# Optimization experiments

Measured on AMD Instinct MI355X. Metric: run time of the kernel, lower is better.

The kernel has to match this reference:

```python
import jax, jax.numpy as jnp
import numpy as np

D_MODEL = 5
NUM_PRED = 3
D_K = D_MODEL + NUM_PRED  # 8
HIDDEN = 128
GRID_LEN = 0.1
NUM_GRIDS = 100  # time_horizon / grid_length
SCALE = float(np.power(D_K, 0.5))
OH = np.eye(NUM_PRED, dtype=np.float32)
ONEHOT_M = jnp.asarray(OH[0])   # mental predicate 0
ONEHOT_A1 = jnp.asarray(OH[1])  # action predicate 1
ONEHOT_A2 = jnp.asarray(OH[2])  # action predicate 2


def time_emb(t):
    # positional-style embedding: even dims sin, odd dims cos (matches fast_time_embedding)
    i = jnp.arange(D_MODEL)
    ang = jnp.asarray(t)[..., None] / (10000.0 ** (2.0 * i / D_MODEL))
    return jnp.where(i % 2 == 0, jnp.sin(ang), jnp.cos(ang))


def setup_inputs() -> dict:
    key = jax.random.key(0)
    ks = jax.random.split(key, 11)
    B, L = 1024, 2048
    times_a1 = jnp.sort(jax.random.uniform(ks[0], (B, L)) * 10.0, axis=1)
    times_a2 = jnp.sort(jax.random.uniform(ks[1], (B, L)) * 10.0, axis=1)
    u = jax.random.uniform(ks[2], (B, NUM_GRIDS))
    s = 0.05
    return {
        'times_a1': times_a1,
        'times_a2': times_a2,
        'u': u,
        'W_ih': s * jax.random.normal(ks[3], (4 * HIDDEN, 21)),
        'W_hh': s * jax.random.normal(ks[4], (4 * HIDDEN, HIDDEN)),
        'b_ih': s * jax.random.normal(ks[5], (4 * HIDDEN,)),
        'b_hh': s * jax.random.normal(ks[6], (4 * HIDDEN,)),
        'w1': s * jax.random.normal(ks[7], (5, HIDDEN)),
        'b1': s * jax.random.normal(ks[8], (5,)),
        'w2': s * jax.random.normal(ks[9], (1, 5)),
        'b2': s * jax.random.normal(ks[10], (1,)),
    }


def _forward(times_a1, times_a2, u, W_ih, W_hh, b_ih, b_hh, w1, b1, w2, b2):
    B = times_a1.shape[0]
    # action event embeddings: [B, L, D_MODEL+NUM_PRED]; k = v = concat over action types
    e1 = jnp.concatenate([time_emb(times_a1), jnp.broadcast_to(ONEHOT_A1, times_a1.shape + (NUM_PRED,))], axis=-1)
    e2 = jnp.concatenate([time_emb(times_a2), jnp.broadcast_to(ONEHOT_A2, times_a2.shape + (NUM_PRED,))], axis=-1)
    kv = jnp.concatenate([e1, e2], axis=1)  # [B, 2L, 8]

    cur_times = (jnp.arange(NUM_GRIDS) + 1.0) * GRID_LEN  # [100]

    def step(carry, xs):
        hx, cx, last_time, has_event, dyn_time = carry
        cur_time, u_t = xs
        # query for mental predicate 0 at cur_time: [8]
        q = jnp.concatenate([time_emb(cur_time), ONEHOT_M])
        scores = jnp.einsum('d,bld->bl', q, kv) / SCALE
        attn = jax.nn.softmax(scores, axis=-1)
        att_out = jnp.einsum('bl,bld->bd', attn, kv)  # [B, 8]
        # mental embedding: zeros before first event, else time-emb of last event + one-hot
        m_emb = jnp.concatenate([time_emb(last_time), jnp.broadcast_to(ONEHOT_M, (B, NUM_PRED))], axis=-1)
        m_emb = jnp.where(has_event[:, None], m_emb, 0.0)
        dyn_time = dyn_time + GRID_LEN
        ct_emb = time_emb(dyn_time)  # [B, 5]
        x = jnp.concatenate([att_out, m_emb, ct_emb], axis=-1)  # [B, 21]
        # torch LSTMCell: gates ordered i, f, g, o
        gates = x @ W_ih.T + hx @ W_hh.T + b_ih + b_hh
        i_, f_, g_, o_ = jnp.split(gates, 4, axis=-1)
        cx = jax.nn.sigmoid(f_) * cx + jax.nn.sigmoid(i_) * jnp.tanh(g_)
        hx = jax.nn.sigmoid(o_) * jnp.tanh(cx)
        hz = jax.nn.sigmoid((hx @ w1.T + b1) @ w2.T + b2)[:, 0]  # [B]
        # bernoulli(prob) with pre-drawn uniform; single mental predicate -> index always 0
        event = u_t < hz
        last_time = jnp.where(event, cur_time, last_time)
        has_event = has_event | event
        dyn_time = jnp.where(event, 0.0, dyn_time)
        return (hx, cx, last_time, has_event, dyn_time), (hz, event)

    init = (
        jnp.zeros((B, HIDDEN)), jnp.zeros((B, HIDDEN)),
        jnp.zeros((B,)), jnp.zeros((B,), dtype=bool), jnp.zeros((B,)),
    )
    _, (hazard, events) = jax.lax.scan(step, init, (cur_times, u.T))
    return hazard, events  # [NUM_GRIDS, B], [NUM_GRIDS, B]


def reference(times_a1, times_a2, u, W_ih, W_hh, b_ih, b_hh, w1, b1, w2, b2):
    return _forward(times_a1, times_a2, u, W_ih, W_hh, b_ih, b_hh, w1, b1, w2, b2)
```

## Files before the change

kernel.cpp:

```cpp
#include <hip/hip_runtime.h>
#include <math.h>

#define BTOT 1024
#define LEN  2048
#define T    100
#define HID  128

#define ATT_OFF_FLOATS 81920

#define C1 0.025118864315095794
#define C2 6.309573444801933e-04
#define C3 1.5848931924611134e-05
#define C4 3.9810717055349735e-07

#define TEMB(td) \
  float d0 = sinf((float)(td)); \
  float d1 = cosf((float)((td) * C1)); \
  float d2 = sinf((float)((td) * C2)); \
  float d3 = cosf((float)((td) * C3)); \
  float d4 = sinf((float)((td) * C4));

__device__ __forceinline__ float sig(float x) { return 1.0f / (1.0f + expf(-x)); }

using v2f = __attribute__((ext_vector_type(2))) float;
__device__ __forceinline__ v2f mkv2(float a, float b) { v2f r; r.x = a; r.y = b; return r; }

template <int CTRL>
__device__ __forceinline__ float dppadd(float x) {
  int r = __builtin_amdgcn_update_dpp(0, __float_as_int(x), CTRL, 0xF, 0xF, false);
  return x + __int_as_float(r);
}
__device__ __forceinline__ float wred(float x) {
  x = dppadd<0xB1>(x);
  x = dppadd<0x4E>(x);
  x = dppadd<0x124>(x);
  x = dppadd<0x128>(x);
  x += __shfl_xor(x, 16);
  x += __shfl_xor(x, 32);
  return x;
}
#define RED8(x) { x = dppadd<0xB1>(x); x = dppadd<0x4E>(x); x = dppadd<0x141>(x); }

__global__ void wprep_k(const float* __restrict__ Wih,
                        const float* __restrict__ Whh,
                        float4* __restrict__ wsT) {
  int i = blockIdx.x * 1024 + threadIdx.x;
  int g = i / 5120;
  int rem = i - g * 5120;
  int c = rem >> 10;
  int t2 = rem & 1023;
  int q = t2 >> 3, s = t2 & 7;
  int row = q + 128 * g;
  int E = 20 * s + 4 * c;
  float v[4];
#pragma unroll
  for (int k = 0; k < 4; k++) {
    int e = E + k;
    v[k] = (e < 21) ? Wih[row * 21 + e]
         : (e < 24) ? 0.f
         : (e < 152) ? Whh[row * HID + (e - 24)]
         : 0.f;
  }
  wsT[i] = make_float4(v[0], v[1], v[2], v[3]);
}

__global__ __attribute__((amdgpu_flat_work_group_size(512, 512)))
void attn_k(const float* __restrict__ ta1,
            const float* __restrict__ ta2,
            float* __restrict__ att) {
  const int b = blockIdx.x, tid = threadIdx.x;
  const int wave = tid >> 6, lane = tid & 63;

  __shared__ float qlds[T][8];
  __shared__ float strip[8][T][8];

  if (tid < T) {
    double ct = (double)(tid + 1) * 0.1;
    TEMB(ct);
    qlds[tid][0] = d0 * 0.35355339059327373f;
    qlds[tid][1] = d1 * 0.35355339059327373f;
    qlds[tid][2] = d2 * 0.35355339059327373f;
    qlds[tid][3] = d3 * 0.35355339059327373f;
    qlds[tid][4] = d4 * 0.35355339059327373f;
  }

#define E5(i) float e##i##_0, e##i##_1, e##i##_2, e##i##_3, e##i##_4;
  E5(0) E5(1) E5(2) E5(3) E5(4) E5(5) E5(6) E5(7)
#undef E5
#define STAGE(i, expr) { double td_ = (double)(expr); \
    e##i##_0 = sinf((float)td_); \
    e##i##_1 = cosf((float)(td_ * C1)); \
    e##i##_2 = sinf((float)(td_ * C2)); \
    e##i##_3 = cosf((float)(td_ * C3)); \
    e##i##_4 = sinf((float)(td_ * C4)); }
  STAGE(0, ta1[b * LEN + tid +    0])
  STAGE(1, ta1[b * LEN + tid +  512])
  STAGE(2, ta1[b * LEN + tid + 1024])
  STAGE(3, ta1[b * LEN + tid + 1536])
  STAGE(4, ta2[b * LEN + tid +    0])
  STAGE(5, ta2[b * LEN + tid +  512])
  STAGE(6, ta2[b * LEN + tid + 1024])
  STAGE(7, ta2[b * LEN + tid + 1536])
#undef STAGE
#define PIN5(i) asm volatile("" : "+v"(e##i##_0), "+v"(e##i##_1), \
    "+v"(e##i##_2), "+v"(e##i##_3), "+v"(e##i##_4));
  PIN5(0) PIN5(1) PIN5(2) PIN5(3) PIN5(4) PIN5(5) PIN5(6) PIN5(7)
#undef PIN5

  __syncthreads();

  for (int t = 0; t < T; t++) {
    const float4 qv = *(const float4*)&qlds[t][0];
    const float q4 = qlds[t][4];
    float Wx = 0.f, Wy = 0.f, Wz = 0.f, Ww = 0.f, W4 = 0.f, sA = 0.f, sB = 0.f;
#define EV(i, S) { \
    float s = fmaf(qv.x, e##i##_0, fmaf(qv.y, e##i##_1, \
              fmaf(qv.z, e##i##_2, fmaf(qv.w, e##i##_3, q4 * e##i##_4)))); \
    float e = __expf(s); S += e; \
    Wx = fmaf(e, e##i##_0, Wx); Wy = fmaf(e, e##i##_1, Wy); \
    Wz = fmaf(e, e##i##_2, Wz); Ww = fmaf(e, e##i##_3, Ww); \
    W4 = fmaf(e, e##i##_4, W4); }
    EV(0, sA) EV(1, sA) EV(2, sA) EV(3, sA)
    EV(4, sB) EV(5, sB) EV(6, sB) EV(7, sB)
#undef EV

    float r0 = wred(Wx), r1 = wred(Wy), r2 = wred(Wz), r3 = wred(Ww);
    float r4 = wred(W4), r5 = wred(sA), r6 = wred(sB);
    if (lane == 0) {
      *(float4*)&strip[wave][t][0] = make_float4(r0, r1, r2, r3);
      strip[wave][t][4] = r4; strip[wave][t][5] = r5; strip[wave][t][6] = r6;
    }
  }
  __syncthreads();

  if (tid < T) {
    float f0 = 0.f, f1 = 0.f, f2 = 0.f, f3 = 0.f, f4 = 0.f, f5 = 0.f, f6 = 0.f;
#pragma unroll
    for (int w = 0; w < 8; w++) {
      float4 a = *(float4*)&strip[w][tid][0];
      float4 bq = *(float4*)&strip[w][tid][4];
      f0 += a.x; f1 += a.y; f2 += a.z; f3 += a.w;
      f4 += bq.x; f5 += bq.y; f6 += bq.z;
    }
    float inv = 1.0f / (f5 + f6);
    float* o8 = &att[(size_t)b * (T * 8) + (size_t)tid * 8];
    o8[0] = f0 * inv; o8[1] = f1 * inv; o8[2] = f2 * inv;
    o8[3] = f3 * inv; o8[4] = f4 * inv;
    o8[5] = 0.f; o8[6] = f5 * inv; o8[7] = f6 * inv;
  }
}

#define XE(tb, b, e) (((tb) * 4 + (b)) * 160 + (e))

__global__ __attribute__((amdgpu_flat_work_group_size(1024, 1024)))
void lstm_k(const float* __restrict__ att,
            const float* __restrict__ u,
            const float4* __restrict__ wT,
            const float* __restrict__ bih,
            const float* __restrict__ bhh,
            const float* __restrict__ w1g,
            const float* __restrict__ b1g,
            const float* __restrict__ w2g,
            const float* __restrict__ b2g,
            float* __restrict__ out) {
  const int tid = threadIdx.x;
  const int bg = blockIdx.x * 4;
  const int s = tid & 7;
  const int q = tid >> 3;
  const int lane = tid & 63;
  const int s5 = s * 5;

  __shared__ float4 xls4[2][4][40];
  __shared__ float4 glds[4][128];
  __shared__ float red2[4][2];
  __shared__ float tembT[101][5];
  __shared__ float uT[4][100];
  __shared__ int stL[2][4], stD[2][4], stH[2][4];
  float* xf = (float*)xls4;

  const int chI = tid & 127;
  float bbc0 = bih[chI] + bhh[chI];
  float bbc1 = bih[chI + 128] + bhh[chI + 128];
  float bbc2 = bih[chI + 256] + bhh[chI + 256];
  float bbc3 = bih[chI + 384] + bhh[chI + 384];
  float wvc = 0.f;
#pragma unroll
  for (int j = 0; j < 5; j++) wvc = fmaf(w2g[j], w1g[j * HID + chI], wvc);
  float hconst = b2g[0];
#pragma unroll
  for (int j = 0; j < 5; j++) hconst = fmaf(w2g[j], b1g[j], hconst);
  asm volatile("" : "+v"(bbc0), "+v"(bbc1), "+v"(bbc2), "+v"(bbc3),
                    "+v"(wvc), "+v"(hconst));
  float cx = 0.f;

  for (int i = tid; i < 2 * 4 * 160; i += 1024) xf[i] = 0.f;
  if (tid < 101) {
    double td = (double)tid * 0.1;
    TEMB(td);
    tembT[tid][0] = d0; tembT[tid][1] = d1; tembT[tid][2] = d2;
    tembT[tid][3] = d3; tembT[tid][4] = d4;
  }
  for (int i = tid; i < 400; i += 1024) {
    int b = i / 100, tt = i - b * 100;
    uT[b][tt] = u[(size_t)(bg + b) * T + tt];
  }
  if (tid < 4) { stL[0][tid] = 0; stD[0][tid] = 0; stH[0][tid] = 0; }
  __syncthreads();

  if (tid < 32) {
    int b = tid >> 3, j = tid & 7;
    xf[XE(0, b, j)] = att[(size_t)(bg + b) * (T * 8) + j];
  } else if (tid >= 64 && tid < 84) {
    int s2 = tid - 64, b = s2 / 5, j = s2 % 5;
    xf[XE(0, b, 16 + j)] = tembT[1][j];
  }
  __syncthreads();

  const float4* wTp = wT;

#define FM1(g, b) \
  a##g##b = __builtin_elementwise_fma(mkv2(w##g.x, w##g.y), xlo, a##g##b); \
  a##g##b = __builtin_elementwise_fma(mkv2(w##g.z, w##g.w), xhi, a##g##b);

#define CHB(b, c) { \
    float4 xb = xls4[tb][b][s5 + (c)]; \
    v2f xlo = mkv2(xb.x, xb.y), xhi = mkv2(xb.z, xb.w); \
    FM1(0, b) FM1(1, b) FM1(2, b) FM1(3, b) }

#define CH(c) { \
    float4 w0 = wTp[(0 * 5 + (c)) * 1024 + tid]; \
    float4 w1 = wTp[(1 * 5 + (c)) * 1024 + tid]; \
    float4 w2 = wTp[(2 * 5 + (c)) * 1024 + tid]; \
    float4 w3 = wTp[(3 * 5 + (c)) * 1024 + tid]; \
    CHB(0, c) CHB(1, c) CHB(2, c) CHB(3, c) }

#define CALCEV(bb) \
    float z_ = hconst + red2[bb][0] + red2[bb][1]; \
    float hz_ = 1.f / (1.f + expf(-z_)); \
    int ev_ = (uT[bb][t] < hz_) ? 1 : 0; \
    int lastp_ = ev_ ? (t + 1) : stL[tb][bb]; \
    int hasp_ = stH[tb][bb] | ev_; \
    int dynp_ = ev_ ? 0 : (stD[tb][bb] + 1);

  for (int t = 0; t < T; t++) {
    const int tb = t & 1, tb1 = tb ^ 1;
    asm volatile("" : "+s"(wTp));

    v2f z2 = mkv2(0.f, 0.f);
    v2f a00 = z2, a01 = z2, a02 = z2, a03 = z2,
        a10 = z2, a11 = z2, a12 = z2, a13 = z2,
        a20 = z2, a21 = z2, a22 = z2, a23 = z2,
        a30 = z2, a31 = z2, a32 = z2, a33 = z2;
    CH(0) CH(1) CH(2) CH(3) CH(4)

    float h00 = a00.x + a00.y, h01 = a01.x + a01.y, h02 = a02.x + a02.y, h03 = a03.x + a03.y;
    float h10 = a10.x + a10.y, h11 = a11.x + a11.y, h12 = a12.x + a12.y, h13 = a13.x + a13.y;
    float h20 = a20.x + a20.y, h21 = a21.x + a21.y, h22 = a22.x + a22.y, h23 = a23.x + a23.y;
    float h30 = a30.x + a30.y, h31 = a31.x + a31.y, h32 = a32.x + a32.y, h33 = a33.x + a33.y;
    RED8(h00) RED8(h01) RED8(h02) RED8(h03)
    RED8(h10) RED8(h11) RED8(h12) RED8(h13)
    RED8(h20) RED8(h21) RED8(h22) RED8(h23)
    RED8(h30) RED8(h31) RED8(h32) RED8(h33)
    if (s == 0) {
      glds[0][q] = make_float4(h00, h10, h20, h30);
      glds[1][q] = make_float4(h01, h11, h21, h31);
      glds[2][q] = make_float4(h02, h12, h22, h32);
      glds[3][q] = make_float4(h03, h13, h23, h33);
    }
    __syncthreads();

    if (tid < 512) {
      int b = tid >> 7;
      float4 g4 = glds[b][chI];
      float gi = g4.x + bbc0, gf = g4.y + bbc1, gG = g4.z + bbc2, go = g4.w + bbc3;
      cx = sig(gf) * cx + sig(gi) * tanhf(gG);
      float hn = sig(go) * tanhf(cx);
      xf[XE(tb1, b, 24 + chI)] = hn;
      float pb = wred(wvc * hn);
      if (lane == 0) red2[b][(tid >> 6) & 1] = pb;
    }
    __syncthreads();

    if (tid < 4) {
      int b = tid;
      CALCEV(b);
      out[(size_t)t * BTOT + bg + b] = hz_;
      out[(size_t)T * BTOT + (size_t)t * BTOT + bg + b] = ev_ ? 1.f : 0.f;
      stL[tb1][b] = lastp_; stH[tb1][b] = hasp_; stD[tb1][b] = dynp_;
    }
    if (t < T - 1) {
      if (tid < 32) {
        int b = tid >> 3, j = tid & 7;
        xf[XE(tb1, b, j)] = att[(size_t)(bg + b) * (T * 8) + (size_t)(t + 1) * 8 + j];
      } else if (tid < 52) {
        int s2 = tid - 32, b = s2 / 5, j = s2 % 5;
        CALCEV(b);
        xf[XE(tb1, b, 8 + j)] = hasp_ ? tembT[lastp_][j] : 0.f;
      } else if (tid < 64) {
        int s2 = tid - 52, b = s2 / 3, j = s2 % 3;
        CALCEV(b);
        xf[XE(tb1, b, 13 + j)] = (j == 0 && hasp_) ? 1.f : 0.f;
      } else if (tid < 84) {
        int s2 = tid - 64, b = s2 / 5, j = s2 % 5;
        CALCEV(b);
        xf[XE(tb1, b, 16 + j)] = tembT[dynp_ + 1][j];
      }
    }
    __syncthreads();
  }
#undef CALCEV
#undef CH
#undef CHB
#undef FM1
}

extern "C" void kernel_launch(void* const* d_in, const int* in_sizes, int n_in,
                              void* d_out, int out_size, void* d_ws, size_t ws_size,
                              hipStream_t stream) {
  const float* ta1 = (const float*)d_in[0];
  const float* ta2 = (const float*)d_in[1];
  const float* u   = (const float*)d_in[2];
  const float* Wih = (const float*)d_in[3];
  const float* Whh = (const float*)d_in[4];
  const float* bih = (const float*)d_in[5];
  const float* bhh = (const float*)d_in[6];
  const float* w1  = (const float*)d_in[7];
  const float* b1  = (const float*)d_in[8];
  const float* w2  = (const float*)d_in[9];
  const float* b2  = (const float*)d_in[10];
  float* out = (float*)d_out;
  float4* wsT = (float4*)d_ws;
  float* att = (float*)d_ws + ATT_OFF_FLOATS;

  wprep_k<<<dim3(20), dim3(1024), 0, stream>>>(Wih, Whh, wsT);
  attn_k<<<dim3(BTOT), dim3(512), 0, stream>>>(ta1, ta2, att);
  lstm_k<<<dim3(BTOT / 4), dim3(1024), 0, stream>>>(att, u, wsT, bih, bhh,
                                                    w1, b1, w2, b2, out);
}
```

Measured before the change: 835.2 us.

## Keep LSTM weights resident in AGPRs, halve block size, drop weight-prep kernel

The LSTM kernel now runs 512 threads per block, each covering 40 input elements instead of 20, and loads its slice of W_ih/W_hh once into accumulation registers (AGPRs) via inline asm. This removes the per-timestep global/L2 weight reloads and the separate weight transpose kernel. The reduction across lanes shrinks from 8 to 4. The cost is 160 AGPRs per thread and a read instruction per weight use, plus lower occupancy from register pressure.

```diff
diff --git a/kernel.cpp b/kernel.cpp
--- a/kernel.cpp
+++ b/kernel.cpp
@@ -5,8 +5,6 @@
 #define LEN  2048
 #define T    100
 #define HID  128
-
-#define ATT_OFF_FLOATS 81920
 
 #define C1 0.025118864315095794
 #define C2 6.309573444801933e-04
@@ -39,30 +37,10 @@
   x += __shfl_xor(x, 32);
   return x;
 }
-#define RED8(x) { x = dppadd<0xB1>(x); x = dppadd<0x4E>(x); x = dppadd<0x141>(x); }
-
-__global__ void wprep_k(const float* __restrict__ Wih,
-                        const float* __restrict__ Whh,
-                        float4* __restrict__ wsT) {
-  int i = blockIdx.x * 1024 + threadIdx.x;
-  int g = i / 5120;
-  int rem = i - g * 5120;
-  int c = rem >> 10;
-  int t2 = rem & 1023;
-  int q = t2 >> 3, s = t2 & 7;
-  int row = q + 128 * g;
-  int E = 20 * s + 4 * c;
-  float v[4];
-#pragma unroll
-  for (int k = 0; k < 4; k++) {
-    int e = E + k;
-    v[k] = (e < 21) ? Wih[row * 21 + e]
-         : (e < 24) ? 0.f
-         : (e < 152) ? Whh[row * HID + (e - 24)]
-         : 0.f;
-  }
-  wsT[i] = make_float4(v[0], v[1], v[2], v[3]);
-}
+#define RED4(x) { x = dppadd<0xB1>(x); x = dppadd<0x4E>(x); }
+
+#define AGSTASH(a_, v_) asm volatile("v_accvgpr_write_b32 %0, %1" : "=a"(a_) : "v"(v_))
+#define AGREAD(v_, a_)  asm volatile("v_accvgpr_read_b32 %0, %1" : "=v"(v_) : "a"(a_))
 
 __global__ __attribute__((amdgpu_flat_work_group_size(512, 512)))
 void attn_k(const float* __restrict__ ta1,
@@ -152,10 +130,11 @@
 
 #define XE(tb, b, e) (((tb) * 4 + (b)) * 160 + (e))
 
-__global__ __attribute__((amdgpu_flat_work_group_size(1024, 1024)))
+__global__ __attribute__((amdgpu_flat_work_group_size(512, 512), amdgpu_waves_per_eu(2, 4)))
 void lstm_k(const float* __restrict__ att,
             const float* __restrict__ u,
-            const float4* __restrict__ wT,
+            const float* __restrict__ Wih,
+            const float* __restrict__ Whh,
             const float* __restrict__ bih,
             const float* __restrict__ bhh,
             const float* __restrict__ w1g,
@@ -165,10 +144,9 @@
             float* __restrict__ out) {
   const int tid = threadIdx.x;
   const int bg = blockIdx.x * 4;
-  const int s = tid & 7;
-  const int q = tid >> 3;
+  const int q = tid >> 2, s = tid & 3;
   const int lane = tid & 63;
-  const int s5 = s * 5;
+  const int s10 = s * 10;
 
   __shared__ float4 xls4[2][4][40];
   __shared__ float4 glds[4][128];
@@ -177,6 +155,31 @@
   __shared__ float uT[4][100];
   __shared__ int stL[2][4], stD[2][4], stH[2][4];
   float* xf = (float*)xls4;
+
+#define DECL4(g, c) float agw##g##_##c##_0, agw##g##_##c##_1, agw##g##_##c##_2, agw##g##_##c##_3;
+  DECL4(0,0) DECL4(0,1) DECL4(0,2) DECL4(0,3) DECL4(0,4) DECL4(0,5) DECL4(0,6) DECL4(0,7) DECL4(0,8) DECL4(0,9)
+  DECL4(1,0) DECL4(1,1) DECL4(1,2) DECL4(1,3) DECL4(1,4) DECL4(1,5) DECL4(1,6) DECL4(1,7) DECL4(1,8) DECL4(1,9)
+  DECL4(2,0) DECL4(2,1) DECL4(2,2) DECL4(2,3) DECL4(2,4) DECL4(2,5) DECL4(2,6) DECL4(2,7) DECL4(2,8) DECL4(2,9)
+  DECL4(3,0) DECL4(3,1) DECL4(3,2) DECL4(3,3) DECL4(3,4) DECL4(3,5) DECL4(3,6) DECL4(3,7) DECL4(3,8) DECL4(3,9)
+#undef DECL4
+#define LD4(g, c) { \
+    int E_ = 40 * s + 4 * (c); \
+    float4 wv4_; \
+    if (E_ >= 24 && E_ < 152) { \
+      wv4_ = *(const float4*)(Whh + (size_t)(q + 128 * (g)) * HID + (E_ - 24)); \
+    } else if (E_ < 24) { \
+      wv4_.x = (E_ + 0 < 21) ? Wih[(q + 128 * (g)) * 21 + E_ + 0] : 0.f; \
+      wv4_.y = (E_ + 1 < 21) ? Wih[(q + 128 * (g)) * 21 + E_ + 1] : 0.f; \
+      wv4_.z = (E_ + 2 < 21) ? Wih[(q + 128 * (g)) * 21 + E_ + 2] : 0.f; \
+      wv4_.w = (E_ + 3 < 21) ? Wih[(q + 128 * (g)) * 21 + E_ + 3] : 0.f; \
+    } else { wv4_ = make_float4(0.f, 0.f, 0.f, 0.f); } \
+    AGSTASH(agw##g##_##c##_0, wv4_.x); AGSTASH(agw##g##_##c##_1, wv4_.y); \
+    AGSTASH(agw##g##_##c##_2, wv4_.z); AGSTASH(agw##g##_##c##_3, wv4_.w); }
+  LD4(0,0) LD4(0,1) LD4(0,2) LD4(0,3) LD4(0,4) LD4(0,5) LD4(0,6) LD4(0,7) LD4(0,8) LD4(0,9)
+  LD4(1,0) LD4(1,1) LD4(1,2) LD4(1,3) LD4(1,4) LD4(1,5) LD4(1,6) LD4(1,7) LD4(1,8) LD4(1,9)
+  LD4(2,0) LD4(2,1) LD4(2,2) LD4(2,3) LD4(2,4) LD4(2,5) LD4(2,6) LD4(2,7) LD4(2,8) LD4(2,9)
+  LD4(3,0) LD4(3,1) LD4(3,2) LD4(3,3) LD4(3,4) LD4(3,5) LD4(3,6) LD4(3,7) LD4(3,8) LD4(3,9)
+#undef LD4
 
   const int chI = tid & 127;
   float bbc0 = bih[chI] + bhh[chI];
@@ -193,14 +196,14 @@
                     "+v"(wvc), "+v"(hconst));
   float cx = 0.f;
 
-  for (int i = tid; i < 2 * 4 * 160; i += 1024) xf[i] = 0.f;
+  for (int i = tid; i < 2 * 4 * 160; i += 512) xf[i] = 0.f;
   if (tid < 101) {
     double td = (double)tid * 0.1;
     TEMB(td);
     tembT[tid][0] = d0; tembT[tid][1] = d1; tembT[tid][2] = d2;
     tembT[tid][3] = d3; tembT[tid][4] = d4;
   }
-  for (int i = tid; i < 400; i += 1024) {
+  for (int i = tid; i < 400; i += 512) {
     int b = i / 100, tt = i - b * 100;
     uT[b][tt] = u[(size_t)(bg + b) * T + tt];
   }
@@ -216,23 +219,28 @@
   }
   __syncthreads();
 
-  const float4* wTp = wT;
-
-#define FM1(g, b) \
-  a##g##b = __builtin_elementwise_fma(mkv2(w##g.x, w##g.y), xlo, a##g##b); \
-  a##g##b = __builtin_elementwise_fma(mkv2(w##g.z, w##g.w), xhi, a##g##b);
-
-#define CHB(b, c) { \
-    float4 xb = xls4[tb][b][s5 + (c)]; \
-    v2f xlo = mkv2(xb.x, xb.y), xhi = mkv2(xb.z, xb.w); \
-    FM1(0, b) FM1(1, b) FM1(2, b) FM1(3, b) }
+#define GFMA(g, c) { \
+    float t0_, t1_, t2_, t3_; \
+    AGREAD(t0_, agw##g##_##c##_0); AGREAD(t1_, agw##g##_##c##_1); \
+    AGREAD(t2_, agw##g##_##c##_2); AGREAD(t3_, agw##g##_##c##_3); \
+    v2f wlo_ = mkv2(t0_, t1_), whi_ = mkv2(t2_, t3_); \
+    a##g##0 = __builtin_elementwise_fma(wlo_, x0lo, a##g##0); \
+    a##g##0 = __builtin_elementwise_fma(whi_, x0hi, a##g##0); \
+    a##g##1 = __builtin_elementwise_fma(wlo_, x1lo, a##g##1); \
+    a##g##1 = __builtin_elementwise_fma(whi_, x1hi, a##g##1); \
+    a##g##2 = __builtin_elementwise_fma(wlo_, x2lo, a##g##2); \
+    a##g##2 = __builtin_elementwise_fma(whi_, x2hi, a##g##2); \
+    a##g##3 = __builtin_elementwise_fma(wlo_, x3lo, a##g##3); \
+    a##g##3 = __builtin_elementwise_fma(whi_, x3hi, a##g##3); }
 
 #define CH(c) { \
-    float4 w0 = wTp[(0 * 5 + (c)) * 1024 + tid]; \
-    float4 w1 = wTp[(1 * 5 + (c)) * 1024 + tid]; \
-    float4 w2 = wTp[(2 * 5 + (c)) * 1024 + tid]; \
-    float4 w3 = wTp[(3 * 5 + (c)) * 1024 + tid]; \
-    CHB(0, c) CHB(1, c) CHB(2, c) CHB(3, c) }
+    float4 xb0_ = xls4[tb][0][s10 + (c)], xb1_ = xls4[tb][1][s10 + (c)], \
+           xb2_ = xls4[tb][2][s10 + (c)], xb3_ = xls4[tb][3][s10 + (c)]; \
+    v2f x0lo = mkv2(xb0_.x, xb0_.y), x0hi = mkv2(xb0_.z, xb0_.w); \
+    v2f x1lo = mkv2(xb1_.x, xb1_.y), x1hi = mkv2(xb1_.z, xb1_.w); \
+    v2f x2lo = mkv2(xb2_.x, xb2_.y), x2hi = mkv2(xb2_.z, xb2_.w); \
+    v2f x3lo = mkv2(xb3_.x, xb3_.y), x3hi = mkv2(xb3_.z, xb3_.w); \
+    GFMA(0, c) GFMA(1, c) GFMA(2, c) GFMA(3, c) }
 
 #define CALCEV(bb) \
     float z_ = hconst + red2[bb][0] + red2[bb][1]; \
@@ -244,23 +252,22 @@
 
   for (int t = 0; t < T; t++) {
     const int tb = t & 1, tb1 = tb ^ 1;
-    asm volatile("" : "+s"(wTp));
 
     v2f z2 = mkv2(0.f, 0.f);
     v2f a00 = z2, a01 = z2, a02 = z2, a03 = z2,
         a10 = z2, a11 = z2, a12 = z2, a13 = z2,
         a20 = z2, a21 = z2, a22 = z2, a23 = z2,
         a30 = z2, a31 = z2, a32 = z2, a33 = z2;
-    CH(0) CH(1) CH(2) CH(3) CH(4)
+    CH(0) CH(1) CH(2) CH(3) CH(4) CH(5) CH(6) CH(7) CH(8) CH(9)
 
     float h00 = a00.x + a00.y, h01 = a01.x + a01.y, h02 = a02.x + a02.y, h03 = a03.x + a03.y;
     float h10 = a10.x + a10.y, h11 = a11.x + a11.y, h12 = a12.x + a12.y, h13 = a13.x + a13.y;
     float h20 = a20.x + a20.y, h21 = a21.x + a21.y, h22 = a22.x + a22.y, h23 = a23.x + a23.y;
     float h30 = a30.x + a30.y, h31 = a31.x + a31.y, h32 = a32.x + a32.y, h33 = a33.x + a33.y;
-    RED8(h00) RED8(h01) RED8(h02) RED8(h03)
-    RED8(h10) RED8(h11) RED8(h12) RED8(h13)
-    RED8(h20) RED8(h21) RED8(h22) RED8(h23)
-    RED8(h30) RED8(h31) RED8(h32) RED8(h33)
+    RED4(h00) RED4(h01) RED4(h02) RED4(h03)
+    RED4(h10) RED4(h11) RED4(h12) RED4(h13)
+    RED4(h20) RED4(h21) RED4(h22) RED4(h23)
+    RED4(h30) RED4(h31) RED4(h32) RED4(h33)
     if (s == 0) {
       glds[0][q] = make_float4(h00, h10, h20, h30);
       glds[1][q] = make_float4(h01, h11, h21, h31);
@@ -269,7 +276,7 @@
     }
     __syncthreads();
 
-    if (tid < 512) {
+    {
       int b = tid >> 7;
       float4 g4 = glds[b][chI];
       float gi = g4.x + bbc0, gf = g4.y + bbc1, gG = g4.z + bbc2, go = g4.w + bbc3;
@@ -310,8 +317,7 @@
   }
 #undef CALCEV
 #undef CH
-#undef CHB
-#undef FM1
+#undef GFMA
 }
 
 extern "C" void kernel_launch(void* const* d_in, const int* in_sizes, int n_in,
@@ -329,11 +335,9 @@
   const float* w2  = (const float*)d_in[9];
   const float* b2  = (const float*)d_in[10];
   float* out = (float*)d_out;
-  float4* wsT = (float4*)d_ws;
-  float* att = (float*)d_ws + ATT_OFF_FLOATS;
-
-  wprep_k<<<dim3(20), dim3(1024), 0, stream>>>(Wih, Whh, wsT);
+  float* att = (float*)d_ws;
+
   attn_k<<<dim3(BTOT), dim3(512), 0, stream>>>(ta1, ta2, att);
-  lstm_k<<<dim3(BTOT / 4), dim3(1024), 0, stream>>>(att, u, wsT, bih, bhh,
-                                                    w1, b1, w2, b2, out);
-}
+  lstm_k<<<dim3(BTOT / 4), dim3(512), 0, stream>>>(att, u, Wih, Whh, bih, bhh,
+                                                   w1, b1, w2, b2, out);
+}
```

Measured after the change: 729.1 us. -12.7%, faster.
